# Optimization experiments

Measured on AMD Instinct MI355X. Metric: run time of the kernel, lower is better.

The kernel has to match this reference:

```python
import jax, jax.numpy as jnp
import numpy as np

B, N, C, H, BS = 4, 4096, 1024, 16, 64
E = C // H          # head dim = 64
EPS = 1e-3

def setup_inputs() -> dict:
    key = jax.random.key(0)
    k0, k1, k2, k3 = jax.random.split(key, 4)
    x = jax.random.normal(k0, (B, N, C), jnp.float32)
    qkv_w = jax.random.normal(k1, (3 * C, C), jnp.float32) * 0.02
    proj_w = jax.random.normal(k2, (C, C), jnp.float32) * 0.02
    proj_b = jax.random.normal(k3, (C,), jnp.float32) * 0.02
    return {"x": x, "qkv_w": qkv_w, "proj_w": proj_w, "proj_b": proj_b}

def reference(x, qkv_w, proj_w, proj_b):
    b, n, c = x.shape
    h, e, bs = H, E, BS
    u = n // bs  # number of buckets
    # qkv projection (no bias), split to (B,H,N,e) per q/k/v
    qkv = (x @ qkv_w.T).reshape(b, n, 3, h, e).transpose(2, 0, 3, 1, 4)
    q, k, v = qkv[0], qkv[1], qkv[2]
    # feature maps: softmax(q) scaled, exp(k)
    q = jax.nn.softmax(q, axis=-1) * (e ** -0.5)
    k = jnp.exp(k)
    # bucket along sequence: (B,H,U,BS,e)
    b_q = q.reshape(b, h, u, bs, e)
    b_k = k.reshape(b, h, u, bs, e)
    b_v = v.reshape(b, h, u, bs, e)
    # per-bucket k sums and inter-bucket cumulative sums
    b_k_cumsum = jnp.cumsum(b_k.sum(axis=-2), axis=-2)            # (B,H,U,e)
    context = jnp.einsum('bhund,bhune->bhude', b_k, b_v)          # (B,H,U,e,e)
    context = jnp.cumsum(context, axis=2)
    # exclusive shift by one bucket (bucket_size > 1 path in original)
    context = jnp.concatenate(
        [jnp.zeros_like(context[:, :, :1]), context[:, :, :-1]], axis=2)
    b_k_cumsum = jnp.concatenate(
        [jnp.zeros_like(b_k_cumsum[:, :, :1]), b_k_cumsum[:, :, :-1]], axis=2)
    # normalizer, clamped from below at eps
    D_inv = 1.0 / jnp.maximum(
        jnp.einsum('bhud,bhund->bhun', b_k_cumsum, b_q), EPS)
    attn = jnp.einsum('bhund,bhude,bhun->bhune', b_q, context, D_inv)
    out = attn.reshape(b, h, n, e).transpose(0, 2, 1, 3).reshape(b, n, c)
    # output projection (dropouts are identity at eval)
    return out @ proj_w.T + proj_b
```

## Files before the change

kernel.cpp:

```cpp
#include <hip/hip_runtime.h>
#include <stdint.h>


typedef unsigned short u16;
typedef unsigned int u32;
typedef u16   u16x4  __attribute__((ext_vector_type(4)));
typedef u16   u16x8  __attribute__((ext_vector_type(8)));
typedef float f32x4  __attribute__((ext_vector_type(4)));
typedef float float4v __attribute__((ext_vector_type(4)));
typedef __bf16 bf16x8 __attribute__((ext_vector_type(8)));

__device__ __forceinline__ u16 f2bf(float f) {
  return __builtin_bit_cast(u16, (__bf16)f);
}
__device__ __forceinline__ float bf2f(u16 h) {
  return (float)__builtin_bit_cast(__bf16, h);
}

__device__ __forceinline__ void stage16(const u16* g, u16* l) {
  __builtin_amdgcn_global_load_lds(
      (const __attribute__((address_space(1))) u32*)g,
      (__attribute__((address_space(3))) u32*)l, 16, 0, 0);
}

__global__ __launch_bounds__(256) void cvt_all(
    const float* __restrict__ x, const float* __restrict__ wqf,
    const float* __restrict__ wpf, u16* __restrict__ xb,
    u16* __restrict__ wq, u16* __restrict__ wp) {
  int i = blockIdx.x * 256 + threadIdx.x;
  const float* in; u16* out; int j;
  if (i < 4194304)      { in = x;   out = xb; j = i; }
  else if (i < 4980736) { in = wqf; out = wq; j = i - 4194304; }
  else                  { in = wpf; out = wp; j = i - 4980736; }
  float4v v = reinterpret_cast<const float4v*>(in)[j];
  u16x4 o;
  o.x = f2bf(v.x); o.y = f2bf(v.y); o.z = f2bf(v.z); o.w = f2bf(v.w);
  reinterpret_cast<u16x4*>(out)[j] = o;
}

template <int EPI>
__global__ __launch_bounds__(512, 2) void gemm256(
    const u16* __restrict__ A,
    const u16* __restrict__ B,
    const float* __restrict__ bias,
    float* __restrict__ Cf,
    u16* __restrict__ Qf, u16* __restrict__ Kt, u16* __restrict__ Vt,
    int N, int K, int NT) {
  __shared__ u16 As[2][2][256][32];
  __shared__ u16 Bs[2][2][256][32];
  const int tid = threadIdx.x, lane = tid & 63, wave = tid >> 6;
  const int wm = wave >> 2, wn = wave & 3;
  const int l15 = lane & 15, l4 = lane >> 4;
  const int ntn = N >> 8;
  const int cpx = gridDim.x >> 3;
  const int bid = (blockIdx.x & 7) * cpx + (blockIdx.x >> 3);
  const int bm = bid / ntn, bn = bid % ntn;

  const int srow = tid >> 2;
  const int gsl8 = ((tid & 3) ^ ((tid >> 3) & 3)) * 8;
  const u16* Ag = A + (size_t)(bm * 256 + srow) * K + gsl8;
  const u16* Bg = B + (size_t)(bn * 256 + srow) * K + gsl8;
  const size_t rj = (size_t)128 * K;

  const int slotr = (l4 ^ ((l15 >> 1) & 3)) * 8;

  f32x4 acc[8][4] = {};
  bf16x8 a0, a1, a2, a3, a4, a5, a6, a7, b0, b1, b2, b3;

#define STG(P, buf, kh, kt)                                        \
  { const u16* g_ = P##g + (kt) + (kh) * 32;                       \
    stage16(g_,      &P##s[buf][kh][wave * 16][0]);                \
    stage16(g_ + rj, &P##s[buf][kh][128 + wave * 16][0]); }

#define LDA(r0_, r1_, r2_, r3_, kk, mh)                                  \
  { const u16* p_ = &As[cur][kk][wm * 128 + (mh) * 64 + l15][0] + slotr; \
    r0_ = *(const bf16x8*)(p_);                                          \
    r1_ = *(const bf16x8*)(p_ + 512);                                    \
    r2_ = *(const bf16x8*)(p_ + 1024);                                   \
    r3_ = *(const bf16x8*)(p_ + 1536); }

#define LDB(kk)                                                    \
  { const u16* p_ = &Bs[cur][kk][wn * 64 + l15][0] + slotr;        \
    b0 = *(const bf16x8*)(p_);                                     \
    b1 = *(const bf16x8*)(p_ + 512);                               \
    b2 = *(const bf16x8*)(p_ + 1024);                              \
    b3 = *(const bf16x8*)(p_ + 1536); }

#define MM(x, y, z) z = __builtin_amdgcn_mfma_f32_16x16x32_bf16(x, y, z, 0, 0, 0)
#define MFMA16(mb, x0, x1, x2, x3)                                 \
  __builtin_amdgcn_s_setprio(1);                                   \
  MM(x0, b0, acc[(mb) + 0][0]); MM(x0, b1, acc[(mb) + 0][1]);      \
  MM(x0, b2, acc[(mb) + 0][2]); MM(x0, b3, acc[(mb) + 0][3]);      \
  MM(x1, b0, acc[(mb) + 1][0]); MM(x1, b1, acc[(mb) + 1][1]);      \
  MM(x1, b2, acc[(mb) + 1][2]); MM(x1, b3, acc[(mb) + 1][3]);      \
  MM(x2, b0, acc[(mb) + 2][0]); MM(x2, b1, acc[(mb) + 2][1]);      \
  MM(x2, b2, acc[(mb) + 2][2]); MM(x2, b3, acc[(mb) + 2][3]);      \
  MM(x3, b0, acc[(mb) + 3][0]); MM(x3, b1, acc[(mb) + 3][1]);      \
  MM(x3, b2, acc[(mb) + 3][2]); MM(x3, b3, acc[(mb) + 3][3]);      \
  __builtin_amdgcn_s_setprio(0);

#define BARF()                                                     \
  { asm volatile("" ::: "memory");                                 \
    __builtin_amdgcn_s_barrier();                                  \
    asm volatile("" ::: "memory"); }

  STG(A, 0, 0, 0) STG(B, 0, 0, 0) STG(A, 0, 1, 0) STG(B, 0, 1, 0)
  asm volatile("s_waitcnt vmcnt(0)" ::: "memory");
  __builtin_amdgcn_s_barrier();
  asm volatile("" ::: "memory");

  for (int t = 0; t < NT; ++t) {
    const int cur = t & 1, nxt = cur ^ 1;
    const int ktn = (t + 1) << 6;
    const bool pre = (t + 1 < NT);
    LDB(0)
    LDA(a0, a1, a2, a3, 0, 0)
    LDA(a4, a5, a6, a7, 0, 1)
    if (pre) STG(A, nxt, 0, ktn)
    MFMA16(0, a0, a1, a2, a3)
    if (pre) STG(B, nxt, 0, ktn)
    MFMA16(4, a4, a5, a6, a7)
    if (pre) { asm volatile("s_waitcnt vmcnt(4)" ::: "memory"); }
    else     { asm volatile("s_waitcnt vmcnt(0)" ::: "memory"); }
    BARF()
    LDB(1)
    LDA(a0, a1, a2, a3, 1, 0)
    LDA(a4, a5, a6, a7, 1, 1)
    if (pre) STG(A, nxt, 1, ktn)
    MFMA16(0, a0, a1, a2, a3)
    if (pre) STG(B, nxt, 1, ktn)
    MFMA16(4, a4, a5, a6, a7)
    if (pre) { asm volatile("s_waitcnt vmcnt(4)" ::: "memory"); }
    BARF()
  }
#undef STG
#undef LDA
#undef LDB
#undef MM
#undef MFMA16
#undef BARF

  const int row0 = bm * 256 + wm * 128 + l4 * 4;
  const int col0 = bn * 256 + wn * 64 + l15;
  if constexpr (EPI == 0) {
    float bv[4];
#pragma unroll
    for (int ni = 0; ni < 4; ++ni) bv[ni] = bias[col0 + ni * 16];
#pragma unroll
    for (int mi = 0; mi < 8; ++mi)
#pragma unroll
      for (int i = 0; i < 4; ++i) {
        size_t r = (size_t)(row0 + mi * 16 + i) * N;
#pragma unroll
        for (int ni = 0; ni < 4; ++ni)
          Cf[r + col0 + ni * 16] = acc[mi][ni][i] + bv[ni];
      }
  } else {
    const int i3 = bn >> 2;
    const int h  = ((bn & 3) << 2) + wn;
    if (i3 == 0) {
#pragma unroll
      for (int mi = 0; mi < 8; ++mi)
#pragma unroll
        for (int i = 0; i < 4; ++i) {
          const int row = row0 + mi * 16 + i;
          const int bb = row >> 12, uu = (row >> 6) & 63, nn = row & 63;
          u16* op = Qf + ((size_t)((bb * 16 + h) * 64 + uu)) * 4096
                        + nn * 64 + l15;
          float v0 = acc[mi][0][i], v1 = acc[mi][1][i];
          float v2 = acc[mi][2][i], v3 = acc[mi][3][i];
          float mx = fmaxf(fmaxf(v0, v1), fmaxf(v2, v3));
          mx = fmaxf(mx, __shfl_xor(mx, 1));
          mx = fmaxf(mx, __shfl_xor(mx, 2));
          mx = fmaxf(mx, __shfl_xor(mx, 4));
          mx = fmaxf(mx, __shfl_xor(mx, 8));
          float e0 = __expf(v0 - mx), e1 = __expf(v1 - mx);
          float e2 = __expf(v2 - mx), e3 = __expf(v3 - mx);
          float s = e0 + e1 + e2 + e3;
          s += __shfl_xor(s, 1); s += __shfl_xor(s, 2);
          s += __shfl_xor(s, 4); s += __shfl_xor(s, 8);
          float inv = 0.125f / s;
          op[0]  = f2bf(e0 * inv); op[16] = f2bf(e1 * inv);
          op[32] = f2bf(e2 * inv); op[48] = f2bf(e3 * inv);
        }
    } else {
      u16* dst = (i3 == 1) ? Kt : Vt;
#pragma unroll
      for (int mi = 0; mi < 8; ++mi) {
        const int row = row0 + mi * 16;
        const int bb = row >> 12, uu = (row >> 6) & 63, nn = row & 63;
        u16* op = dst + ((size_t)((bb * 16 + h) * 64 + uu)) * 4096 + nn;
#pragma unroll
        for (int ni = 0; ni < 4; ++ni) {
          const int d = ni * 16 + l15;
          u16x4 o;
          if (i3 == 1) {
            o.x = f2bf(__expf(acc[mi][ni][0]));
            o.y = f2bf(__expf(acc[mi][ni][1]));
            o.z = f2bf(__expf(acc[mi][ni][2]));
            o.w = f2bf(__expf(acc[mi][ni][3]));
          } else {
            o.x = f2bf(acc[mi][ni][0]); o.y = f2bf(acc[mi][ni][1]);
            o.z = f2bf(acc[mi][ni][2]); o.w = f2bf(acc[mi][ni][3]);
          }
          *reinterpret_cast<u16x4*>(op + d * 64) = o;
        }
      }
    }
  }
}

__global__ __launch_bounds__(256) void buildctx(
    const u16* __restrict__ Kt,
    const u16* __restrict__ Vt,
    u16* __restrict__ ctxb, float* __restrict__ ksum) {
  const int bid = blockIdx.x;
  const int tid = threadIdx.x, lane = tid & 63, wave = tid >> 6;
  const int l15 = lane & 15, l4 = lane >> 4;
  __shared__ float dp[64][4];
  const size_t base = (size_t)bid * 4096;

  {
    int d = tid >> 2, c = tid & 3;
    const u16* kp = Kt + base + d * 64 + c * 16;
    float a = 0.f;
#pragma unroll
    for (int j = 0; j < 16; ++j) a += bf2f(kp[j]);
    dp[d][c] = a;
  }

  f32x4 acc[4] = {};
#pragma unroll
  for (int kk = 0; kk < 2; ++kk) {
    bf16x8 av = *reinterpret_cast<const bf16x8*>(
        Vt + base + (wave * 16 + l15) * 64 + kk * 32 + l4 * 8);
#pragma unroll
    for (int ni = 0; ni < 4; ++ni) {
      bf16x8 bk = *reinterpret_cast<const bf16x8*>(
          Kt + base + (ni * 16 + l15) * 64 + kk * 32 + l4 * 8);
      acc[ni] = __builtin_amdgcn_mfma_f32_16x16x32_bf16(av, bk, acc[ni], 0, 0, 0);
    }
  }
  __syncthreads();
  if (tid < 64)
    ksum[(size_t)bid * 64 + tid] = dp[tid][0] + dp[tid][1] + dp[tid][2] + dp[tid][3];
  u16* cb = ctxb + base;
#pragma unroll
  for (int ni = 0; ni < 4; ++ni)
#pragma unroll
    for (int i = 0; i < 4; ++i)
      cb[(wave * 16 + l4 * 4 + i) * 64 + ni * 16 + l15] = f2bf(acc[ni][i]);
}

__global__ __launch_bounds__(256) void scanctx(
    u16* __restrict__ ctxb, float* __restrict__ ksum) {
  const int bh = blockIdx.x >> 2, c = blockIdx.x & 3;
  const int tid = threadIdx.x;
  u16* p = ctxb + (size_t)bh * 64 * 4096 + c * 1024 + tid * 4;
  float* kp = ksum + (size_t)bh * 64 * 64 + tid;
  const bool dok = (c == 0) && (tid < 64);

  float r0 = 0.f, r1 = 0.f, r2 = 0.f, r3 = 0.f, runk = 0.f;
#define LC(i) (*reinterpret_cast<const u16x4*>(p + (size_t)(i) * 4096))
#define LK(i) (dok ? kp[(size_t)(i) * 64] : 0.f)
  u16x4 c0 = LC(0), c1 = LC(1), c2 = LC(2), c3 = LC(3);
  float k0 = LK(0), k1 = LK(1), k2 = LK(2), k3 = LK(3);
  for (int u = 0; u < 64; u += 4) {
    const int i4 = u + 4 < 64 ? u + 4 : 63, i5 = u + 5 < 64 ? u + 5 : 63;
    const int i6 = u + 6 < 64 ? u + 6 : 63, i7 = u + 7 < 64 ? u + 7 : 63;
    u16x4 n0 = LC(i4), n1 = LC(i5), n2 = LC(i6), n3 = LC(i7);
    float m0 = LK(i4), m1 = LK(i5), m2 = LK(i6), m3 = LK(i7);
#define STEP(idx, cv, kv)                                                  \
    {                                                                      \
      u16x4 o;                                                             \
      o.x = f2bf(r0); o.y = f2bf(r1); o.z = f2bf(r2); o.w = f2bf(r3);      \
      *reinterpret_cast<u16x4*>(p + (size_t)(idx) * 4096) = o;             \
      if (dok) kp[(size_t)(idx) * 64] = runk;                              \
      r0 += bf2f(cv.x); r1 += bf2f(cv.y); r2 += bf2f(cv.z);                \
      r3 += bf2f(cv.w); runk += kv;                                        \
    }
    STEP(u, c0, k0) STEP(u + 1, c1, k1) STEP(u + 2, c2, k2) STEP(u + 3, c3, k3)
#undef STEP
    c0 = n0; c1 = n1; c2 = n2; c3 = n3;
    k0 = m0; k1 = m1; k2 = m2; k3 = m3;
  }
#undef LC
#undef LK
}

__global__ __launch_bounds__(256) void apply(
    const u16* __restrict__ Q, const u16* __restrict__ ctxc,
    const float* __restrict__ kcum, u16* __restrict__ AT) {
  const int bid = blockIdx.x;
  const int u = bid & 63, bh = bid >> 6, b = bh >> 4, h = bh & 15;
  const int tid = threadIdx.x, lane = tid & 63, wave = tid >> 6;
  const int l15 = lane & 15, l4 = lane >> 4;
  __shared__ float kc[64];
  __shared__ float dp[64][4];
  __shared__ float dinv[64];

  const size_t base = (size_t)bid * 4096;
  const u16* Qu = Q + base;
  if (tid < 64) kc[tid] = kcum[(size_t)bid * 64 + tid];
  __syncthreads();
  {
    int n = tid & 63, q = tid >> 6;
    const u16* qp = Qu + n * 64 + q * 16;
    float a = 0.f;
#pragma unroll
    for (int j = 0; j < 16; ++j) a += bf2f(qp[j]) * kc[q * 16 + j];
    dp[n][q] = a;
  }
  __syncthreads();
  if (tid < 64)
    dinv[tid] = 1.f / fmaxf(dp[tid][0] + dp[tid][1] + dp[tid][2] + dp[tid][3], 1e-3f);
  __syncthreads();

  f32x4 acc[4] = {};
  const u16* Cu = ctxc + base;
#pragma unroll
  for (int kk = 0; kk < 2; ++kk) {
    bf16x8 aq = *reinterpret_cast<const bf16x8*>(Qu + (wave * 16 + l15) * 64 + kk * 32 + l4 * 8);
#pragma unroll
    for (int ni = 0; ni < 4; ++ni) {
      bf16x8 bc = *reinterpret_cast<const bf16x8*>(Cu + (ni * 16 + l15) * 64 + kk * 32 + l4 * 8);
      acc[ni] = __builtin_amdgcn_mfma_f32_16x16x32_bf16(aq, bc, acc[ni], 0, 0, 0);
    }
  }
  const size_t orow = ((size_t)b * 4096 + u * 64 + wave * 16 + l4 * 4) * 1024 + h * 64;
#pragma unroll
  for (int i = 0; i < 4; ++i) {
    float di = dinv[wave * 16 + l4 * 4 + i];
#pragma unroll
    for (int ni = 0; ni < 4; ++ni)
      AT[orow + (size_t)i * 1024 + ni * 16 + l15] = f2bf(acc[ni][i] * di);
  }
}

extern "C" void kernel_launch(void* const* d_in, const int* in_sizes, int n_in,
                              void* d_out, int out_size, void* d_ws, size_t ws_size,
                              hipStream_t stream) {
  (void)in_sizes; (void)n_in; (void)out_size; (void)ws_size;
  const float* x      = (const float*)d_in[0];
  const float* qkv_w  = (const float*)d_in[1];
  const float* proj_w = (const float*)d_in[2];
  const float* proj_b = (const float*)d_in[3];
  float* out = (float*)d_out;

  char* ws = (char*)d_ws;
  u16* xb    = (u16*)(ws);
  u16* wq    = (u16*)(ws + 33554432);
  u16* wp    = (u16*)(ws + 39845888);
  u16* Qf    = (u16*)(ws + 41943040);
  u16* Kt    = (u16*)(ws + 75497472);
  u16* Vt    = (u16*)(ws + 109051904);
  u16* ctxb  = (u16*)(ws + 142606336);
  float* ksum = (float*)(ws + 176160768);
  u16* AT    = Kt;

  cvt_all<<<dim3(20480), dim3(256), 0, stream>>>(x, qkv_w, proj_w, xb, wq, wp);

  gemm256<2><<<dim3(64 * 12), dim3(512), 0, stream>>>(
      xb, wq, nullptr, nullptr, Qf, Kt, Vt, 3072, 1024, 16);
  buildctx<<<dim3(4096), dim3(256), 0, stream>>>(Kt, Vt, ctxb, ksum);
  scanctx<<<dim3(256), dim3(256), 0, stream>>>(ctxb, ksum);
  apply<<<dim3(4096), dim3(256), 0, stream>>>(Qf, ctxb, ksum, AT);
  gemm256<0><<<dim3(64 * 4), dim3(512), 0, stream>>>(
      AT, wp, proj_b, out, nullptr, nullptr, nullptr, 1024, 1024, 16);
}
```

Before: 249.1 us.

## Fuse K-sum into QKV GEMM epilogue and merge context build with scan

The per-bucket sum of exp(K) moves into the QKV GEMM epilogue, using wave shuffles and direct stores, which removes that reduction from a separate kernel. The buildctx and scanctx kernels become one scanctx2 kernel that walks the buckets in order, computes each bucket's K^T V with MFMA and carries the running prefix in registers. This avoids writing and re-reading the per-bucket context. A small scanK kernel does the exclusive scan of the K sums. The serial loop over 64 buckets gives only 256 blocks with one MFMA accumulator each, so latency and low parallelism may limit the fused scan.

```diff
diff --git a/kernel.cpp b/kernel.cpp
--- a/kernel.cpp
+++ b/kernel.cpp
@@ -45,6 +45,7 @@
     const float* __restrict__ bias,
     float* __restrict__ Cf,
     u16* __restrict__ Qf, u16* __restrict__ Kt, u16* __restrict__ Vt,
+    float* __restrict__ ksum,
     int N, int K, int NT) {
   __shared__ u16 As[2][2][256][32];
   __shared__ u16 Bs[2][2][256][32];
@@ -61,7 +62,6 @@
   const u16* Ag = A + (size_t)(bm * 256 + srow) * K + gsl8;
   const u16* Bg = B + (size_t)(bn * 256 + srow) * K + gsl8;
   const size_t rj = (size_t)128 * K;
-
   const int slotr = (l4 ^ ((l15 >> 1) & 3)) * 8;
 
   f32x4 acc[8][4] = {};
@@ -183,108 +183,132 @@
           op[0]  = f2bf(e0 * inv); op[16] = f2bf(e1 * inv);
           op[32] = f2bf(e2 * inv); op[48] = f2bf(e3 * inv);
         }
-    } else {
-      u16* dst = (i3 == 1) ? Kt : Vt;
+    } else if (i3 == 1) {
+      float sk0[4] = {0.f, 0.f, 0.f, 0.f};
+      float sk1[4] = {0.f, 0.f, 0.f, 0.f};
 #pragma unroll
       for (int mi = 0; mi < 8; ++mi) {
         const int row = row0 + mi * 16;
         const int bb = row >> 12, uu = (row >> 6) & 63, nn = row & 63;
-        u16* op = dst + ((size_t)((bb * 16 + h) * 64 + uu)) * 4096 + nn;
+        u16* op = Kt + ((size_t)((bb * 16 + h) * 64 + uu)) * 4096 + nn;
 #pragma unroll
         for (int ni = 0; ni < 4; ++ni) {
-          const int d = ni * 16 + l15;
+          float e0 = __expf(acc[mi][ni][0]);
+          float e1 = __expf(acc[mi][ni][1]);
+          float e2 = __expf(acc[mi][ni][2]);
+          float e3 = __expf(acc[mi][ni][3]);
           u16x4 o;
-          if (i3 == 1) {
-            o.x = f2bf(__expf(acc[mi][ni][0]));
-            o.y = f2bf(__expf(acc[mi][ni][1]));
-            o.z = f2bf(__expf(acc[mi][ni][2]));
-            o.w = f2bf(__expf(acc[mi][ni][3]));
-          } else {
-            o.x = f2bf(acc[mi][ni][0]); o.y = f2bf(acc[mi][ni][1]);
-            o.z = f2bf(acc[mi][ni][2]); o.w = f2bf(acc[mi][ni][3]);
-          }
-          *reinterpret_cast<u16x4*>(op + d * 64) = o;
+          o.x = f2bf(e0); o.y = f2bf(e1); o.z = f2bf(e2); o.w = f2bf(e3);
+          *reinterpret_cast<u16x4*>(op + (ni * 16 + l15) * 64) = o;
+          if (mi < 4) sk0[ni] += e0 + e1 + e2 + e3;
+          else        sk1[ni] += e0 + e1 + e2 + e3;
         }
       }
-    }
-  }
-}
-
-__global__ __launch_bounds__(256) void buildctx(
+#pragma unroll
+      for (int ni = 0; ni < 4; ++ni) {
+        sk0[ni] += __shfl_xor(sk0[ni], 16); sk0[ni] += __shfl_xor(sk0[ni], 32);
+        sk1[ni] += __shfl_xor(sk1[ni], 16); sk1[ni] += __shfl_xor(sk1[ni], 32);
+      }
+      if (lane < 16) {
+        const int nb0 = bm * 256 + wm * 128;
+        const size_t bkt0 = (size_t)(((nb0 >> 12) * 16 + h) * 64 + ((nb0 >> 6) & 63));
+#pragma unroll
+        for (int ni = 0; ni < 4; ++ni) {
+          ksum[bkt0 * 64 + ni * 16 + l15]       = sk0[ni];
+          ksum[(bkt0 + 1) * 64 + ni * 16 + l15] = sk1[ni];
+        }
+      }
+    } else {
+#pragma unroll
+      for (int mi = 0; mi < 8; ++mi) {
+        const int row = row0 + mi * 16;
+        const int bb = row >> 12, uu = (row >> 6) & 63, nn = row & 63;
+        u16* op = Vt + ((size_t)((bb * 16 + h) * 64 + uu)) * 4096 + nn;
+#pragma unroll
+        for (int ni = 0; ni < 4; ++ni) {
+          u16x4 o;
+          o.x = f2bf(acc[mi][ni][0]); o.y = f2bf(acc[mi][ni][1]);
+          o.z = f2bf(acc[mi][ni][2]); o.w = f2bf(acc[mi][ni][3]);
+          *reinterpret_cast<u16x4*>(op + (ni * 16 + l15) * 64) = o;
+        }
+      }
+    }
+  }
+}
+
+__global__ __launch_bounds__(256) void scanctx2(
     const u16* __restrict__ Kt,
     const u16* __restrict__ Vt,
-    u16* __restrict__ ctxb, float* __restrict__ ksum) {
-  const int bid = blockIdx.x;
+    u16* __restrict__ ctxb) {
+  const int bh = blockIdx.x >> 2, ec = blockIdx.x & 3;
   const int tid = threadIdx.x, lane = tid & 63, wave = tid >> 6;
   const int l15 = lane & 15, l4 = lane >> 4;
-  __shared__ float dp[64][4];
-  const size_t base = (size_t)bid * 4096;
-
-  {
-    int d = tid >> 2, c = tid & 3;
-    const u16* kp = Kt + base + d * 64 + c * 16;
-    float a = 0.f;
-#pragma unroll
-    for (int j = 0; j < 16; ++j) a += bf2f(kp[j]);
-    dp[d][c] = a;
-  }
-
-  f32x4 acc[4] = {};
-#pragma unroll
-  for (int kk = 0; kk < 2; ++kk) {
-    bf16x8 av = *reinterpret_cast<const bf16x8*>(
-        Vt + base + (wave * 16 + l15) * 64 + kk * 32 + l4 * 8);
-#pragma unroll
-    for (int ni = 0; ni < 4; ++ni) {
-      bf16x8 bk = *reinterpret_cast<const bf16x8*>(
-          Kt + base + (ni * 16 + l15) * 64 + kk * 32 + l4 * 8);
-      acc[ni] = __builtin_amdgcn_mfma_f32_16x16x32_bf16(av, bk, acc[ni], 0, 0, 0);
-    }
-  }
+  __shared__ u16 KtL[2][64][72];
+  __shared__ u16 VtL[2][16][72];
+
+  const size_t bbase = (size_t)bh * 64 * 4096;
+  const int kr0 = tid >> 3, ks0 = (tid & 7) * 8;
+  const int kr1 = 32 + kr0;
+  const bool dov = tid < 128;
+  const int vr = tid >> 3, vs = (tid & 7) * 8;
+
+  f32x4 acc = {0.f, 0.f, 0.f, 0.f};
+
+  u16x8 k0 = *reinterpret_cast<const u16x8*>(Kt + bbase + kr0 * 64 + ks0);
+  u16x8 k1 = *reinterpret_cast<const u16x8*>(Kt + bbase + kr1 * 64 + ks0);
+  u16x8 v0 = {};
+  if (dov) v0 = *reinterpret_cast<const u16x8*>(Vt + bbase + (ec * 16 + vr) * 64 + vs);
+  *reinterpret_cast<u16x8*>(&KtL[0][kr0][ks0]) = k0;
+  *reinterpret_cast<u16x8*>(&KtL[0][kr1][ks0]) = k1;
+  if (dov) *reinterpret_cast<u16x8*>(&VtL[0][vr][vs]) = v0;
   __syncthreads();
-  if (tid < 64)
-    ksum[(size_t)bid * 64 + tid] = dp[tid][0] + dp[tid][1] + dp[tid][2] + dp[tid][3];
-  u16* cb = ctxb + base;
-#pragma unroll
-  for (int ni = 0; ni < 4; ++ni)
-#pragma unroll
-    for (int i = 0; i < 4; ++i)
-      cb[(wave * 16 + l4 * 4 + i) * 64 + ni * 16 + l15] = f2bf(acc[ni][i]);
-}
-
-__global__ __launch_bounds__(256) void scanctx(
-    u16* __restrict__ ctxb, float* __restrict__ ksum) {
-  const int bh = blockIdx.x >> 2, c = blockIdx.x & 3;
-  const int tid = threadIdx.x;
-  u16* p = ctxb + (size_t)bh * 64 * 4096 + c * 1024 + tid * 4;
-  float* kp = ksum + (size_t)bh * 64 * 64 + tid;
-  const bool dok = (c == 0) && (tid < 64);
-
-  float r0 = 0.f, r1 = 0.f, r2 = 0.f, r3 = 0.f, runk = 0.f;
-#define LC(i) (*reinterpret_cast<const u16x4*>(p + (size_t)(i) * 4096))
-#define LK(i) (dok ? kp[(size_t)(i) * 64] : 0.f)
-  u16x4 c0 = LC(0), c1 = LC(1), c2 = LC(2), c3 = LC(3);
-  float k0 = LK(0), k1 = LK(1), k2 = LK(2), k3 = LK(3);
+
+  for (int u = 0; u < 64; ++u) {
+    const int cur = u & 1, nxt = cur ^ 1;
+    const bool pre = (u + 1 < 64);
+    if (pre) {
+      const size_t nb = bbase + (size_t)(u + 1) * 4096;
+      k0 = *reinterpret_cast<const u16x8*>(Kt + nb + kr0 * 64 + ks0);
+      k1 = *reinterpret_cast<const u16x8*>(Kt + nb + kr1 * 64 + ks0);
+      if (dov) v0 = *reinterpret_cast<const u16x8*>(Vt + nb + (ec * 16 + vr) * 64 + vs);
+    }
+    {
+      u16* cb = ctxb + (bbase + (size_t)u * 4096) + wave * 16 + l15;
+#pragma unroll
+      for (int i = 0; i < 4; ++i)
+        cb[(ec * 16 + l4 * 4 + i) * 64] = f2bf(acc[i]);
+    }
+#pragma unroll
+    for (int kk = 0; kk < 2; ++kk) {
+      bf16x8 av = *reinterpret_cast<const bf16x8*>(&VtL[cur][l15][kk * 32 + l4 * 8]);
+      bf16x8 bk = *reinterpret_cast<const bf16x8*>(&KtL[cur][wave * 16 + l15][kk * 32 + l4 * 8]);
+      acc = __builtin_amdgcn_mfma_f32_16x16x32_bf16(av, bk, acc, 0, 0, 0);
+    }
+    if (pre) {
+      *reinterpret_cast<u16x8*>(&KtL[nxt][kr0][ks0]) = k0;
+      *reinterpret_cast<u16x8*>(&KtL[nxt][kr1][ks0]) = k1;
+      if (dov) *reinterpret_cast<u16x8*>(&VtL[nxt][vr][vs]) = v0;
+    }
+    __syncthreads();
+  }
+}
+
+__global__ __launch_bounds__(64) void scanK(float* __restrict__ ksum) {
+  const int bh = blockIdx.x;
+  float* p = ksum + (size_t)bh * 4096 + threadIdx.x;
+  float run = 0.f;
+#define LK(i) p[(size_t)(i) * 64]
+  float c0 = LK(0), c1 = LK(1), c2 = LK(2), c3 = LK(3);
   for (int u = 0; u < 64; u += 4) {
     const int i4 = u + 4 < 64 ? u + 4 : 63, i5 = u + 5 < 64 ? u + 5 : 63;
     const int i6 = u + 6 < 64 ? u + 6 : 63, i7 = u + 7 < 64 ? u + 7 : 63;
-    u16x4 n0 = LC(i4), n1 = LC(i5), n2 = LC(i6), n3 = LC(i7);
-    float m0 = LK(i4), m1 = LK(i5), m2 = LK(i6), m3 = LK(i7);
-#define STEP(idx, cv, kv)                                                  \
-    {                                                                      \
-      u16x4 o;                                                             \
-      o.x = f2bf(r0); o.y = f2bf(r1); o.z = f2bf(r2); o.w = f2bf(r3);      \
-      *reinterpret_cast<u16x4*>(p + (size_t)(idx) * 4096) = o;             \
-      if (dok) kp[(size_t)(idx) * 64] = runk;                              \
-      r0 += bf2f(cv.x); r1 += bf2f(cv.y); r2 += bf2f(cv.z);                \
-      r3 += bf2f(cv.w); runk += kv;                                        \
-    }
-    STEP(u, c0, k0) STEP(u + 1, c1, k1) STEP(u + 2, c2, k2) STEP(u + 3, c3, k3)
-#undef STEP
+    float n0 = LK(i4), n1 = LK(i5), n2 = LK(i6), n3 = LK(i7);
+    LK(u) = run;     run += c0;
+    LK(u + 1) = run; run += c1;
+    LK(u + 2) = run; run += c2;
+    LK(u + 3) = run; run += c3;
     c0 = n0; c1 = n1; c2 = n2; c3 = n3;
-    k0 = m0; k1 = m1; k2 = m2; k3 = m3;
-  }
-#undef LC
+  }
 #undef LK
 }
 
@@ -361,10 +385,10 @@
   cvt_all<<<dim3(20480), dim3(256), 0, stream>>>(x, qkv_w, proj_w, xb, wq, wp);
 
   gemm256<2><<<dim3(64 * 12), dim3(512), 0, stream>>>(
-      xb, wq, nullptr, nullptr, Qf, Kt, Vt, 3072, 1024, 16);
-  buildctx<<<dim3(4096), dim3(256), 0, stream>>>(Kt, Vt, ctxb, ksum);
-  scanctx<<<dim3(256), dim3(256), 0, stream>>>(ctxb, ksum);
+      xb, wq, nullptr, nullptr, Qf, Kt, Vt, ksum, 3072, 1024, 16);
+  scanK<<<dim3(64), dim3(64), 0, stream>>>(ksum);
+  scanctx2<<<dim3(256), dim3(256), 0, stream>>>(Kt, Vt, ctxb);
   apply<<<dim3(4096), dim3(256), 0, stream>>>(Qf, ctxb, ksum, AT);
   gemm256<0><<<dim3(64 * 4), dim3(512), 0, stream>>>(
-      AT, wp, proj_b, out, nullptr, nullptr, nullptr, 1024, 1024, 16);
-}
+      AT, wp, proj_b, out, nullptr, nullptr, nullptr, nullptr, 1024, 1024, 16);
+}
```

Result: faster. 240.6 us (-3.4%).
